# Performance work log

Measured on AMD Instinct MI355X. Metric: run time of the kernel, lower is better.

The kernel has to match this reference:

```python
import jax, jax.numpy as jnp
import numpy as np

HEADS = 8
EPS = 1e-5


def _layernorm(x, g, b):
    mu = jnp.mean(x, axis=-1, keepdims=True)
    var = jnp.mean(jnp.square(x - mu), axis=-1, keepdims=True)
    return (x - mu) * jax.lax.rsqrt(var + EPS) * g + b


def setup_inputs() -> dict:
    key = jax.random.key(0)
    ks = jax.random.split(key, 10)
    B, S, D = 4, 2048, 256
    d_ff = 2 * D
    s = 0.02
    return {
        "x": jax.random.normal(ks[0], (B, S, D), dtype=jnp.float32),
        "ln1_g": jnp.ones((D,), jnp.float32),
        "ln1_b": jnp.zeros((D,), jnp.float32),
        "w_qkv": jax.random.normal(ks[1], (3 * D, D), jnp.float32) * s,
        "b_qkv": jnp.zeros((3 * D,), jnp.float32),
        "w_proj": jax.random.normal(ks[2], (D, D), jnp.float32) * s,
        "b_proj": jnp.zeros((D,), jnp.float32),
        "ln2_g": jnp.ones((D,), jnp.float32),
        "ln2_b": jnp.zeros((D,), jnp.float32),
        "w1": jax.random.normal(ks[3], (d_ff, D), jnp.float32) * s,
        "b1": jnp.zeros((d_ff,), jnp.float32),
        "w2": jax.random.normal(ks[4], (D, d_ff), jnp.float32) * s,
        "b2": jnp.zeros((D,), jnp.float32),
    }


def reference(x, ln1_g, ln1_b, w_qkv, b_qkv, w_proj, b_proj,
              ln2_g, ln2_b, w1, b1, w2, b2):
    B, S, D = x.shape
    H = HEADS
    dh = D // H
    scale = dh ** -0.5

    # --- attention sublayer (pre-LN) ---
    y = _layernorm(x, ln1_g, ln1_b)
    qkv = y @ w_qkv.T + b_qkv                       # [B,S,3D]
    qkv = qkv.reshape(B, S, 3, H, dh)
    q = jnp.transpose(qkv[:, :, 0], (0, 2, 1, 3))   # [B,H,S,dh]
    k = jnp.transpose(qkv[:, :, 1], (0, 2, 1, 3))
    v = jnp.transpose(qkv[:, :, 2], (0, 2, 1, 3))
    attn = jax.nn.softmax(jnp.einsum('bhsd,bhtd->bhst', q, k) * scale, axis=-1)
    ctx = jnp.einsum('bhst,bhtd->bhsd', attn, v)    # [B,H,S,dh]
    ctx = jnp.transpose(ctx, (0, 2, 1, 3)).reshape(B, S, D)
    x = x + ctx @ w_proj.T + b_proj

    # --- FFN sublayer (pre-LN) ---
    y = _layernorm(x, ln2_g, ln2_b)
    h = jax.nn.silu(y @ w1.T + b1)                  # [B,S,2D]
    x = x + h @ w2.T + b2
    return x
```

## Files before the change

### kernel.cpp

```cpp
#include <hip/hip_runtime.h>
#include <cstddef>

constexpr int kB   = 4;
constexpr int kS   = 2048;
constexpr int kD   = 256;
constexpr int kH   = 8;
constexpr int kDH  = 32;
constexpr int kDFF = 512;
constexpr int kM   = kB * kS;
constexpr float kEps = 1e-5f;
constexpr float kScaleL2E = 0.17677669529663687f * 1.4426950408889634f;

typedef float f32x4  __attribute__((ext_vector_type(4)));
typedef short bf16x8 __attribute__((ext_vector_type(8)));
typedef unsigned short u16;
typedef unsigned int   u32;

__device__ inline u16 f2bf(float x) {
    union { float f; unsigned u; } c; c.f = x;
    const unsigned r = c.u + 0x7fffu + ((c.u >> 16) & 1u);
    return (u16)(r >> 16);
}

__device__ inline u32 pk_trunc(float lo, float hi) {
    union { float f; u32 u; } a, b; a.f = lo; b.f = hi;
    return __builtin_amdgcn_perm(b.u, a.u, 0x07060302u);
}

__global__ __launch_bounds__(256)
void conv_w_kernel(const float* __restrict__ wq, const float* __restrict__ wp,
                   const float* __restrict__ w1, const float* __restrict__ w2,
                   u16* __restrict__ dst)
{
    const int e0 = (blockIdx.x * 256 + threadIdx.x) * 4;
    const float* src;
    int off;
    if (e0 < 196608)      { src = wq; off = e0; }
    else if (e0 < 262144) { src = wp; off = e0 - 196608; }
    else if (e0 < 393216) { src = w1; off = e0 - 262144; }
    else                  { src = w2; off = e0 - 393216; }
    const float4 v = *(const float4*)&src[off];
    *(ushort4*)&dst[e0] = make_ushort4(f2bf(v.x), f2bf(v.y), f2bf(v.z), f2bf(v.w));
}

__global__ __launch_bounds__(256)
void ln_kernel(const float* __restrict__ x, const float* __restrict__ g,
               const float* __restrict__ b, u16* __restrict__ y)
{
    const int wave = threadIdx.x >> 6;
    const int lane = threadIdx.x & 63;
    const int row  = blockIdx.x * 4 + wave;
    const float4 v = *(const float4*)&x[(size_t)row * kD + lane * 4];
    float s1 = (v.x + v.y) + (v.z + v.w);
    float s2 = (v.x * v.x + v.y * v.y) + (v.z * v.z + v.w * v.w);
    #pragma unroll
    for (int off = 1; off < 64; off <<= 1) {
        s1 += __shfl_xor(s1, off);
        s2 += __shfl_xor(s2, off);
    }
    const float mu  = s1 * (1.0f / kD);
    const float var = s2 * (1.0f / kD) - mu * mu;
    const float inv = rsqrtf(var + kEps);
    const float4 g4 = *(const float4*)&g[lane * 4];
    const float4 b4 = *(const float4*)&b[lane * 4];
    *(ushort4*)&y[(size_t)row * kD + lane * 4] = make_ushort4(
        f2bf((v.x - mu) * inv * g4.x + b4.x),
        f2bf((v.y - mu) * inv * g4.y + b4.y),
        f2bf((v.z - mu) * inv * g4.z + b4.z),
        f2bf((v.w - mu) * inv * g4.w + b4.w));
}

template<int NT, int OUTMODE, bool RES, int KTOT>
__global__ __launch_bounds__(256)
void gemm_direct(const u16* __restrict__ A, const u16* __restrict__ Wb,
                 const float* __restrict__ bias, const float* __restrict__ res,
                 float* __restrict__ Cf, u16* __restrict__ Cb,
                 u16* __restrict__ KbP, u16* __restrict__ VtP, int N)
{
    constexpr int NI = NT / 16;
    constexpr int NK = KTOT / 32;
    const int tid  = threadIdx.x;
    const int wave = tid >> 6;
    const int lane = tid & 63;
    const int quad = lane >> 4;
    const int l16  = lane & 15;
    const int m0 = blockIdx.x * 128;
    const int n0 = blockIdx.y * NT;

    f32x4 acc[2][NI];
    #pragma unroll
    for (int mt = 0; mt < 2; ++mt)
        #pragma unroll
        for (int ni = 0; ni < NI; ++ni) acc[mt][ni] = {0.f, 0.f, 0.f, 0.f};

    const u16* arow0 = &A[(size_t)(m0 + wave * 16 + l16) * KTOT + quad * 8];
    const u16* arow1 = &A[(size_t)(m0 + 64 + wave * 16 + l16) * KTOT + quad * 8];
    const u16* wrow  = &Wb[(size_t)(n0 + l16) * KTOT + quad * 8];

    #pragma unroll 2
    for (int k = 0; k < NK; ++k) {
        const bf16x8 a0 = *(const bf16x8*)&arow0[k * 32];
        const bf16x8 a1 = *(const bf16x8*)&arow1[k * 32];
        #pragma unroll
        for (int ni = 0; ni < NI; ++ni) {
            const bf16x8 wf = *(const bf16x8*)&wrow[(size_t)ni * 16 * KTOT + k * 32];
            acc[0][ni] = __builtin_amdgcn_mfma_f32_16x16x32_bf16(a0, wf, acc[0][ni], 0, 0, 0);
            acc[1][ni] = __builtin_amdgcn_mfma_f32_16x16x32_bf16(a1, wf, acc[1][ni], 0, 0, 0);
        }
    }

    #pragma unroll
    for (int mt = 0; mt < 2; ++mt) {
        #pragma unroll
        for (int ni = 0; ni < NI; ++ni) {
            const float bias_v = bias[n0 + ni * 16 + l16];
            #pragma unroll
            for (int r = 0; r < 4; ++r) {
                const int m = m0 + mt * 64 + wave * 16 + quad * 4 + r;
                float v = acc[mt][ni][r] + bias_v;
                if (OUTMODE == 0) {
                    const int n = n0 + ni * 16 + l16;
                    if (RES) v += res[(size_t)m * N + n];
                    Cf[(size_t)m * N + n] = v;
                } else if (OUTMODE == 1) {
                    const int n = n0 + ni * 16 + l16;
                    v = v / (1.0f + __expf(-v));
                    Cb[(size_t)m * N + n] = f2bf(v);
                } else {
                    const int rgn = n0 >> 8;
                    const int nl  = (n0 & 255) + ni * 16 + l16;
                    const int hh  = nl >> 5, dh = nl & 31;
                    const int bb  = m >> 11, s = m & (kS - 1);
                    const int bh  = bb * kH + hh;
                    if (rgn == 0)
                        Cb[((size_t)bh * kS + s) * kDH + dh] = f2bf(v * kScaleL2E);
                    else if (rgn == 1)
                        KbP[((size_t)bh * kS + s) * kDH + dh] = f2bf(v);
                    else {
                        const int so = s & 31;
                        const int vq = (so >> 2) & 3;
                        const int vj = (so & 3) | (((so >> 4) & 1) << 2);
                        VtP[(((size_t)bh * (kS / 32) + (s >> 5)) * 4 + vq) * 256
                            + dh * 8 + vj] = f2bf(v);
                    }
                }
            }
        }
    }
}

__global__ __launch_bounds__(256)
void attn_kernel(const u16* __restrict__ Qb, const u16* __restrict__ Kb,
                 const u16* __restrict__ Vp, u16* __restrict__ ctx)
{
    __shared__ float cbuf[2][64 * 33];
    const int tid  = threadIdx.x;
    const int wave = tid >> 6;
    const int lane = tid & 63;
    const int quad = lane >> 4;
    const int l16  = lane & 15;
    const int h = blockIdx.y;
    const int b = blockIdx.z;
    const int bh = b * kH + h;
    const int qsub = wave >> 1;
    const int half = wave & 1;
    const int q0 = blockIdx.x * 128 + qsub * 64;

    bf16x8 aq[4];
    #pragma unroll
    for (int qb = 0; qb < 4; ++qb)
        aq[qb] = *(const bf16x8*)
            &Qb[((size_t)bh * kS + q0 + qb * 16 + l16) * kDH + quad * 8];

    const u16* Kbase = Kb + (size_t)bh * kS * kDH;
    const u16* Vbase = Vp + (size_t)bh * (kS * 32);

    f32x4 O[4][2] = {};
    f32x4 lsum[4] = {};
    const f32x4 zz = {0.f, 0.f, 0.f, 0.f};
    union { u32 u[4]; bf16x8 v; } ones;
    ones.u[0] = ones.u[1] = ones.u[2] = ones.u[3] = 0x3F803F80u;

    auto load_tile = [&](int kt, bf16x8 (&kf)[4], bf16x8 (&vf)[2][2]) {
        #pragma unroll
        for (int kg = 0; kg < 4; ++kg)
            kf[kg] = *(const bf16x8*)
                &Kbase[(size_t)(kt + kg * 16 + l16) * kDH + quad * 8];
        #pragma unroll
        for (int ks = 0; ks < 2; ++ks)
            #pragma unroll
            for (int nf = 0; nf < 2; ++nf)
                vf[ks][nf] = *(const bf16x8*)
                    &Vbase[(size_t)(((kt >> 5) + ks) * 4 + quad) * 1024
                           + (nf * 16 + l16) * 8];
    };

    auto comp_tile = [&](bf16x8 (&kf)[4], bf16x8 (&vf)[2][2]) {
        #pragma unroll
        for (int qb = 0; qb < 4; ++qb) {
            f32x4 S0 = __builtin_amdgcn_mfma_f32_16x16x32_bf16(kf[0], aq[qb], zz, 0, 0, 0);
            f32x4 S1 = __builtin_amdgcn_mfma_f32_16x16x32_bf16(kf[1], aq[qb], zz, 0, 0, 0);
            f32x4 S2 = __builtin_amdgcn_mfma_f32_16x16x32_bf16(kf[2], aq[qb], zz, 0, 0, 0);
            f32x4 S3 = __builtin_amdgcn_mfma_f32_16x16x32_bf16(kf[3], aq[qb], zz, 0, 0, 0);

            union { u32 u[4]; bf16x8 v; } pA0, pA1;
            pA0.u[0] = pk_trunc(__builtin_amdgcn_exp2f(S0[0]), __builtin_amdgcn_exp2f(S0[1]));
            pA0.u[1] = pk_trunc(__builtin_amdgcn_exp2f(S0[2]), __builtin_amdgcn_exp2f(S0[3]));
            pA0.u[2] = pk_trunc(__builtin_amdgcn_exp2f(S1[0]), __builtin_amdgcn_exp2f(S1[1]));
            pA0.u[3] = pk_trunc(__builtin_amdgcn_exp2f(S1[2]), __builtin_amdgcn_exp2f(S1[3]));
            pA1.u[0] = pk_trunc(__builtin_amdgcn_exp2f(S2[0]), __builtin_amdgcn_exp2f(S2[1]));
            pA1.u[1] = pk_trunc(__builtin_amdgcn_exp2f(S2[2]), __builtin_amdgcn_exp2f(S2[3]));
            pA1.u[2] = pk_trunc(__builtin_amdgcn_exp2f(S3[0]), __builtin_amdgcn_exp2f(S3[1]));
            pA1.u[3] = pk_trunc(__builtin_amdgcn_exp2f(S3[2]), __builtin_amdgcn_exp2f(S3[3]));

            lsum[qb] = __builtin_amdgcn_mfma_f32_16x16x32_bf16(pA0.v, ones.v, lsum[qb], 0, 0, 0);
            lsum[qb] = __builtin_amdgcn_mfma_f32_16x16x32_bf16(pA1.v, ones.v, lsum[qb], 0, 0, 0);

            O[qb][0] = __builtin_amdgcn_mfma_f32_16x16x32_bf16(pA0.v, vf[0][0], O[qb][0], 0, 0, 0);
            O[qb][1] = __builtin_amdgcn_mfma_f32_16x16x32_bf16(pA0.v, vf[0][1], O[qb][1], 0, 0, 0);
            O[qb][0] = __builtin_amdgcn_mfma_f32_16x16x32_bf16(pA1.v, vf[1][0], O[qb][0], 0, 0, 0);
            O[qb][1] = __builtin_amdgcn_mfma_f32_16x16x32_bf16(pA1.v, vf[1][1], O[qb][1], 0, 0, 0);
        }
    };

    const int kbeg = half * (kS / 2);
    #pragma unroll 1
    for (int t2 = 0; t2 < 8; ++t2) {
        const int ktA = kbeg + t2 * 128;
        bf16x8 kfA[4], vfA[2][2], kfB[4], vfB[2][2];
        load_tile(ktA,      kfA, vfA);
        load_tile(ktA + 64, kfB, vfB);
        comp_tile(kfA, vfA);
        comp_tile(kfB, vfB);
    }

    float* cb = cbuf[qsub];
    if (half == 1) {
        #pragma unroll
        for (int qb = 0; qb < 4; ++qb)
            #pragma unroll
            for (int r = 0; r < 4; ++r) {
                const int row = qb * 16 + quad * 4 + r;
                cb[row * 33 + l16]      = O[qb][0][r];
                cb[row * 33 + 16 + l16] = O[qb][1][r];
                if (l16 == 0)
                    cb[row * 33 + 32] = lsum[qb][r];
            }
    }
    __syncthreads();
    if (half == 0) {
        #pragma unroll
        for (int qb = 0; qb < 4; ++qb)
            #pragma unroll
            for (int r = 0; r < 4; ++r) {
                const int row = qb * 16 + quad * 4 + r;
                const float lq  = lsum[qb][r] + cb[row * 33 + 32];
                const float inv = 1.0f / lq;
                const float o0 = O[qb][0][r] + cb[row * 33 + l16];
                const float o1 = O[qb][1][r] + cb[row * 33 + 16 + l16];
                const int q = q0 + row;
                u16* crow = ctx + ((size_t)(b * kS + q)) * kD + h * kDH;
                crow[l16]      = f2bf(o0 * inv);
                crow[16 + l16] = f2bf(o1 * inv);
            }
    }
}

extern "C" void kernel_launch(void* const* d_in, const int* in_sizes, int n_in,
                              void* d_out, int out_size, void* d_ws, size_t ws_size,
                              hipStream_t stream)
{
    const float* x      = (const float*)d_in[0];
    const float* ln1_g  = (const float*)d_in[1];
    const float* ln1_b  = (const float*)d_in[2];
    const float* w_qkv  = (const float*)d_in[3];
    const float* b_qkv  = (const float*)d_in[4];
    const float* w_proj = (const float*)d_in[5];
    const float* b_proj = (const float*)d_in[6];
    const float* ln2_g  = (const float*)d_in[7];
    const float* ln2_b  = (const float*)d_in[8];
    const float* w1     = (const float*)d_in[9];
    const float* b1     = (const float*)d_in[10];
    const float* w2     = (const float*)d_in[11];
    const float* b2     = (const float*)d_in[12];
    float* out = (float*)d_out;

    char* ws = (char*)d_ws;
    u16* Qb  = (u16*)ws;
    u16* Kb  = (u16*)(ws + ((size_t)4  << 20));
    u16* Vp  = (u16*)(ws + ((size_t)8  << 20));
    u16* ctx = (u16*)(ws + ((size_t)12 << 20));
    u16* y   = (u16*)(ws + ((size_t)16 << 20));
    u16* h   = (u16*)ws;
    u16* Wb  = (u16*)(ws + ((size_t)20 << 20));
    u16* wqb = Wb;
    u16* wpb = Wb + 196608;
    u16* w1b = Wb + 262144;
    u16* w2b = Wb + 393216;

    const dim3 blk(256);

    conv_w_kernel<<<dim3(512), blk, 0, stream>>>(w_qkv, w_proj, w1, w2, Wb);
    ln_kernel<<<dim3(kM / 4), blk, 0, stream>>>(x, ln1_g, ln1_b, y);
    gemm_direct<64, 2, false, 256><<<dim3(kM / 128, 12), blk, 0, stream>>>(
        y, wqb, b_qkv, nullptr, nullptr, Qb, Kb, Vp, 0);
    attn_kernel<<<dim3(kS / 128, kH, kB), blk, 0, stream>>>(Qb, Kb, Vp, ctx);
    gemm_direct<32, 0, true, 256><<<dim3(kM / 128, kD / 32), blk, 0, stream>>>(
        ctx, wpb, b_proj, x, out, nullptr, nullptr, nullptr, kD);
    ln_kernel<<<dim3(kM / 4), blk, 0, stream>>>(out, ln2_g, ln2_b, y);
    gemm_direct<64, 1, false, 256><<<dim3(kM / 128, kDFF / 64), blk, 0, stream>>>(
        y, w1b, b1, nullptr, nullptr, h, nullptr, nullptr, kDFF);
    gemm_direct<32, 0, true, 512><<<dim3(kM / 128, kD / 32), blk, 0, stream>>>(
        h, w2b, b2, out, out, nullptr, nullptr, nullptr, kD);
}
```

Measured before the change: 183.5 us.

## Store GEMM operands in MFMA-fragment packed tiles for contiguous loads

Weights, layernorm outputs, attention context and FFN hidden activations are now written in a packed 16x32 tile layout, with each tile stored contiguously. The GEMM kernel can then read each wavefront's bf16x8 fragment as one contiguous 1 KB chunk instead of 16 strided rows. This is meant to improve coalescing and cut cache-line waste on the direct-from-global operand loads. The cost is scattered index arithmetic and less contiguous writes in the producer kernels (LN, attention epilogue, SiLU epilogue).

```diff
diff --git a/kernel.cpp b/kernel.cpp
--- a/kernel.cpp
+++ b/kernel.cpp
@@ -27,20 +27,26 @@
     return __builtin_amdgcn_perm(b.u, a.u, 0x07060302u);
 }
 
+__device__ inline size_t pkoff(int row, int col, int nkb) {
+    return ((size_t)(row >> 4) * nkb + (col >> 5)) * 512
+         + (row & 15) * 32 + (col & 31);
+}
+
 __global__ __launch_bounds__(256)
 void conv_w_kernel(const float* __restrict__ wq, const float* __restrict__ wp,
                    const float* __restrict__ w1, const float* __restrict__ w2,
                    u16* __restrict__ dst)
 {
     const int e0 = (blockIdx.x * 256 + threadIdx.x) * 4;
-    const float* src;
-    int off;
-    if (e0 < 196608)      { src = wq; off = e0; }
-    else if (e0 < 262144) { src = wp; off = e0 - 196608; }
-    else if (e0 < 393216) { src = w1; off = e0 - 262144; }
-    else                  { src = w2; off = e0 - 393216; }
+    const float* src; int off, K, base;
+    if (e0 < 196608)      { src = wq; off = e0;          K = 256; base = 0; }
+    else if (e0 < 262144) { src = wp; off = e0 - 196608; K = 256; base = 196608; }
+    else if (e0 < 393216) { src = w1; off = e0 - 262144; K = 256; base = 262144; }
+    else                  { src = w2; off = e0 - 393216; K = 512; base = 393216; }
     const float4 v = *(const float4*)&src[off];
-    *(ushort4*)&dst[e0] = make_ushort4(f2bf(v.x), f2bf(v.y), f2bf(v.z), f2bf(v.w));
+    const int n = off / K, k = off - n * K;
+    const size_t po = pkoff(n, k, K >> 5);
+    *(ushort4*)&dst[base + po] = make_ushort4(f2bf(v.x), f2bf(v.y), f2bf(v.z), f2bf(v.w));
 }
 
 __global__ __launch_bounds__(256)
@@ -63,21 +69,20 @@
     const float inv = rsqrtf(var + kEps);
     const float4 g4 = *(const float4*)&g[lane * 4];
     const float4 b4 = *(const float4*)&b[lane * 4];
-    *(ushort4*)&y[(size_t)row * kD + lane * 4] = make_ushort4(
+    *(ushort4*)&y[pkoff(row, lane * 4, kD >> 5)] = make_ushort4(
         f2bf((v.x - mu) * inv * g4.x + b4.x),
         f2bf((v.y - mu) * inv * g4.y + b4.y),
         f2bf((v.z - mu) * inv * g4.z + b4.z),
         f2bf((v.w - mu) * inv * g4.w + b4.w));
 }
 
-template<int NT, int OUTMODE, bool RES, int KTOT>
+template<int NI, int OUTMODE, bool RES, int KTOT>
 __global__ __launch_bounds__(256)
-void gemm_direct(const u16* __restrict__ A, const u16* __restrict__ Wb,
-                 const float* __restrict__ bias, const float* __restrict__ res,
-                 float* __restrict__ Cf, u16* __restrict__ Cb,
-                 u16* __restrict__ KbP, u16* __restrict__ VtP, int N)
-{
-    constexpr int NI = NT / 16;
+void gemm_pk(const u16* __restrict__ Ap, const u16* __restrict__ Wp,
+             const float* __restrict__ bias, const float* __restrict__ res,
+             float* __restrict__ Cf, u16* __restrict__ Cb,
+             u16* __restrict__ KbP, u16* __restrict__ VtP, int N)
+{
     constexpr int NK = KTOT / 32;
     const int tid  = threadIdx.x;
     const int wave = tid >> 6;
@@ -85,7 +90,8 @@
     const int quad = lane >> 4;
     const int l16  = lane & 15;
     const int m0 = blockIdx.x * 128;
-    const int n0 = blockIdx.y * NT;
+    const int n0 = blockIdx.y * (NI * 16);
+    const int fo = l16 * 32 + quad * 8;
 
     f32x4 acc[2][NI];
     #pragma unroll
@@ -93,17 +99,17 @@
         #pragma unroll
         for (int ni = 0; ni < NI; ++ni) acc[mt][ni] = {0.f, 0.f, 0.f, 0.f};
 
-    const u16* arow0 = &A[(size_t)(m0 + wave * 16 + l16) * KTOT + quad * 8];
-    const u16* arow1 = &A[(size_t)(m0 + 64 + wave * 16 + l16) * KTOT + quad * 8];
-    const u16* wrow  = &Wb[(size_t)(n0 + l16) * KTOT + quad * 8];
+    const u16* a0p = Ap + (size_t)((m0 >> 4) + wave)     * NK * 512 + fo;
+    const u16* a1p = Ap + (size_t)((m0 >> 4) + 4 + wave) * NK * 512 + fo;
+    const u16* wp  = Wp + (size_t)(n0 >> 4)              * NK * 512 + fo;
 
     #pragma unroll 2
     for (int k = 0; k < NK; ++k) {
-        const bf16x8 a0 = *(const bf16x8*)&arow0[k * 32];
-        const bf16x8 a1 = *(const bf16x8*)&arow1[k * 32];
+        const bf16x8 a0 = *(const bf16x8*)&a0p[k * 512];
+        const bf16x8 a1 = *(const bf16x8*)&a1p[k * 512];
         #pragma unroll
         for (int ni = 0; ni < NI; ++ni) {
-            const bf16x8 wf = *(const bf16x8*)&wrow[(size_t)ni * 16 * KTOT + k * 32];
+            const bf16x8 wf = *(const bf16x8*)&wp[((size_t)ni * NK + k) * 512];
             acc[0][ni] = __builtin_amdgcn_mfma_f32_16x16x32_bf16(a0, wf, acc[0][ni], 0, 0, 0);
             acc[1][ni] = __builtin_amdgcn_mfma_f32_16x16x32_bf16(a1, wf, acc[1][ni], 0, 0, 0);
         }
@@ -117,18 +123,17 @@
             #pragma unroll
             for (int r = 0; r < 4; ++r) {
                 const int m = m0 + mt * 64 + wave * 16 + quad * 4 + r;
+                const int n = n0 + ni * 16 + l16;
                 float v = acc[mt][ni][r] + bias_v;
                 if (OUTMODE == 0) {
-                    const int n = n0 + ni * 16 + l16;
                     if (RES) v += res[(size_t)m * N + n];
                     Cf[(size_t)m * N + n] = v;
                 } else if (OUTMODE == 1) {
-                    const int n = n0 + ni * 16 + l16;
                     v = v / (1.0f + __expf(-v));
-                    Cb[(size_t)m * N + n] = f2bf(v);
+                    Cb[pkoff(m, n, kDFF >> 5)] = f2bf(v);
                 } else {
                     const int rgn = n0 >> 8;
-                    const int nl  = (n0 & 255) + ni * 16 + l16;
+                    const int nl  = n & 255;
                     const int hh  = nl >> 5, dh = nl & 31;
                     const int bb  = m >> 11, s = m & (kS - 1);
                     const int bh  = bb * kH + hh;
@@ -259,7 +264,9 @@
                 const float o0 = O[qb][0][r] + cb[row * 33 + l16];
                 const float o1 = O[qb][1][r] + cb[row * 33 + 16 + l16];
                 const int q = q0 + row;
-                u16* crow = ctx + ((size_t)(b * kS + q)) * kD + h * kDH;
+                const int mrow = b * kS + q;
+                u16* crow = ctx + ((size_t)(mrow >> 4) * (kD >> 5) + h) * 512
+                          + (mrow & 15) * 32;
                 crow[l16]      = f2bf(o0 * inv);
                 crow[16 + l16] = f2bf(o1 * inv);
             }
@@ -302,14 +309,14 @@
 
     conv_w_kernel<<<dim3(512), blk, 0, stream>>>(w_qkv, w_proj, w1, w2, Wb);
     ln_kernel<<<dim3(kM / 4), blk, 0, stream>>>(x, ln1_g, ln1_b, y);
-    gemm_direct<64, 2, false, 256><<<dim3(kM / 128, 12), blk, 0, stream>>>(
+    gemm_pk<4, 2, false, 256><<<dim3(kM / 128, 12), blk, 0, stream>>>(
         y, wqb, b_qkv, nullptr, nullptr, Qb, Kb, Vp, 0);
     attn_kernel<<<dim3(kS / 128, kH, kB), blk, 0, stream>>>(Qb, Kb, Vp, ctx);
-    gemm_direct<32, 0, true, 256><<<dim3(kM / 128, kD / 32), blk, 0, stream>>>(
+    gemm_pk<2, 0, true, 256><<<dim3(kM / 128, kD / 32), blk, 0, stream>>>(
         ctx, wpb, b_proj, x, out, nullptr, nullptr, nullptr, kD);
     ln_kernel<<<dim3(kM / 4), blk, 0, stream>>>(out, ln2_g, ln2_b, y);
-    gemm_direct<64, 1, false, 256><<<dim3(kM / 128, kDFF / 64), blk, 0, stream>>>(
+    gemm_pk<4, 1, false, 256><<<dim3(kM / 128, kDFF / 64), blk, 0, stream>>>(
         y, w1b, b1, nullptr, nullptr, h, nullptr, nullptr, kDFF);
-    gemm_direct<32, 0, true, 512><<<dim3(kM / 128, kD / 32), blk, 0, stream>>>(
+    gemm_pk<2, 0, true, 512><<<dim3(kM / 128, kD / 32), blk, 0, stream>>>(
         h, w2b, b2, out, out, nullptr, nullptr, nullptr, kD);
 }
```

Result: faster. 162.1 us (-11.7%).
